# Kernel tuning notes

Measured on AMD Instinct MI355X. Metric: run time of the kernel, lower is better.

Reference implementation:

```python
import jax, jax.numpy as jnp
import numpy as np

# Sizes (see shape_source): N samples, D=Config.dim, H=D//2, E question types, C classes/type
N, D, H, E, C = 65536, 768, 384, 8, 8


def setup_inputs() -> dict:
    key = jax.random.key(0)
    k_x, k_t, k_w1, k_w2 = jax.random.split(key, 4)
    x = jax.random.normal(k_x, (N, D), dtype=jnp.float32)
    question_types = jax.random.randint(k_t, (N,), 0, E, dtype=jnp.int32)
    # Stacked per-type MLP head parameters (E experts)
    W1 = jax.random.normal(k_w1, (E, D, H), dtype=jnp.float32) * 0.02
    b1 = jnp.zeros((E, H), dtype=jnp.float32)
    W2 = jax.random.normal(k_w2, (E, H, C), dtype=jnp.float32) * 0.02
    b2 = jnp.zeros((E, C), dtype=jnp.float32)
    return {"x": x, "W1": W1, "b1": b1, "W2": W2, "b2": b2,
            "question_types": question_types}


def reference(x, W1, b1, W2, b2, question_types):
    # Per-sample routed 2-layer MLP head: logits_i = MLP_{type_i}(x_i).
    # Dropout is eval-mode identity. Dense-per-expert compute + mask select
    # (standard MoE reference; E is a small fixed loop, not a data-dim loop).
    n_experts = W1.shape[0]
    out = jnp.zeros((x.shape[0], W2.shape[-1]), dtype=x.dtype)
    for e in range(n_experts):
        h = jax.nn.relu(x @ W1[e] + b1[e])        # [N, H]
        logits = h @ W2[e] + b2[e]                # [N, C]
        out = jnp.where((question_types == e)[:, None], logits, out)
    return out
```

## Files before the change

kernel.cpp:

```cpp
#include <hip/hip_runtime.h>

typedef short s16x8 __attribute__((ext_vector_type(8)));
typedef float f32x4 __attribute__((ext_vector_type(4)));

#define N_SAMPLES 65536
#define DIM 768
#define HID 384
#define NEXP 8
#define NCLS 8
#define JT 24
#define KT 24

#define WS_CNT    0
#define WS_BUCKET 1024
#define WS_W1F    (WS_BUCKET + NEXP * N_SAMPLES * 4)

__device__ __forceinline__ unsigned short f2bf(float f) {
  union { float f; unsigned u; } v; v.f = f;
  unsigned r = v.u + 0x7fffu + ((v.u >> 16) & 1u);
  return (unsigned short)(r >> 16);
}

__device__ __forceinline__ unsigned cvt2(float a, float b) {
  union { float f; unsigned u; } ua, ub;
  ua.f = a; ub.f = b;
  return __builtin_amdgcn_perm(ub.u + 0x8000u, ua.u + 0x8000u, 0x07060302u);
}

#define LBAR asm volatile("s_waitcnt lgkmcnt(0)\n\ts_barrier" ::: "memory")

__global__ void k_w1frag(const float* __restrict__ W1,
                         unsigned short* __restrict__ W1F,
                         int* __restrict__ cnt) {
  if (blockIdx.x == 0 && blockIdx.y == 0 && threadIdx.x < NEXP)
    cnt[threadIdx.x] = 0;
  const int e = blockIdx.x;
  const int unit = blockIdx.y * 4 + (threadIdx.x >> 6);
  const int lane = threadIdx.x & 63;
  const int jt = unit / KT, kt = unit % KT;
  const int j = jt * 16 + (lane & 15);
  const int k0 = kt * 32 + (lane >> 4) * 8;
  const float* src = W1 + ((size_t)e * DIM + k0) * HID + j;
  s16x8 v;
#pragma unroll
  for (int i = 0; i < 8; ++i) v[i] = (short)f2bf(src[(size_t)i * HID]);
  *(s16x8*)&W1F[(((size_t)e * JT * KT + unit) * 64 + lane) * 8] = v;
}

__global__ void k_scatter(const int* __restrict__ qt, int* __restrict__ cnt,
                          int* __restrict__ bucket) {
  __shared__ int lcnt[NEXP], lbase[NEXP];
  const int t = threadIdx.x;
  const int i = blockIdx.x * 256 + t;
  if (t < NEXP) lcnt[t] = 0;
  __syncthreads();
  const int e = qt[i];
  const int rank = atomicAdd(&lcnt[e], 1);
  __syncthreads();
  if (t < NEXP) lbase[t] = atomicAdd(&cnt[t], lcnt[t]);
  __syncthreads();
  bucket[(size_t)e * N_SAMPLES + lbase[e] + rank] = i;
}

#define ALOAD(LO, HI, KS)                                   \
  { const float4* p_ = (const float4*)(ap + (KS) * 32);     \
    LO = p_[0]; HI = p_[1]; }

#define ASTORE(BUF, LO, HI)                                               \
  { unsigned q0 = cvt2((LO).x, (LO).y), q1 = cvt2((LO).z, (LO).w);        \
    unsigned q2 = cvt2((HI).x, (HI).y), q3 = cvt2((HI).z, (HI).w);        \
    uint4 pk_ = {q0, q1, q2, q3};                                         \
    *(uint4*)&(BUF)[ar * 40 + aq * 8] = pk_; }

#define WLOAD(DST, KS)                                                    \
  _Pragma("unroll") for (int ni = 0; ni < 6; ++ni)                        \
      DST[ni] = *(const s16x8*)(wfbase + ((size_t)ni * KT + (KS)) * 512);

#define COMPUTE(AS, WF)                                                   \
  { _Pragma("unroll") for (int mi = 0; mi < 4; ++mi) {                    \
      s16x8 xfr = *(const s16x8*)&(AS)[(mi * 16 + lrow) * 40 + quad * 8]; \
      _Pragma("unroll") for (int ni = 0; ni < 6; ++ni)                    \
          acc[mi][ni] = __builtin_amdgcn_mfma_f32_16x16x32_bf16(          \
              WF[ni], xfr, acc[mi][ni], 0, 0, 0); } }

__global__ __launch_bounds__(256, 2) void k_moe_gemm(
    const float* __restrict__ x, const unsigned short* __restrict__ W1F,
    const float* __restrict__ b1, const float* __restrict__ W2,
    const float* __restrict__ b2, const int* __restrict__ cnt,
    const int* __restrict__ bucket, float* __restrict__ out) {
  __shared__ __align__(16) short smem[25088];
  __shared__ __align__(16) short W2s[16 * 392];
  __shared__ float b1s[HID];
  __shared__ float b2s[NCLS];
  short* As0 = smem;
  short* As1 = smem + 2560;
  short* Hs  = smem;

  const int e = blockIdx.x;
  const int n_e = cnt[e];
  const int t = threadIdx.x;
  const int lane = t & 63;
  const int wave = t >> 6;
  const int lrow = lane & 15;
  const int quad = lane >> 4;
  const int ar = t >> 2;
  const int aq = t & 3;

  for (int j = t; j < HID; j += 256) {
    b1s[j] = b1[e * HID + j];
    const float* wr = W2 + ((size_t)e * HID + j) * NCLS;
#pragma unroll
    for (int c = 0; c < NCLS; ++c) W2s[c * 392 + j] = (short)f2bf(wr[c]);
#pragma unroll
    for (int c = NCLS; c < 16; ++c) W2s[c * 392 + j] = 0;
  }
  if (t < NCLS) b2s[t] = b2[e * NCLS + t];

  const unsigned short* wfbase =
      W1F + ((size_t)(e * JT + wave * 6) * KT) * 512 + lane * 8;

  for (int rt = blockIdx.y; rt * 64 < n_e; rt += gridDim.y) {
    const int row0 = rt * 64;
    int slot = row0 + ar;
    if (slot >= n_e) slot = n_e - 1;
    const int aidx = bucket[(size_t)e * N_SAMPLES + slot];
    const float* ap = x + (size_t)aidx * DIM + aq * 8;

    f32x4 acc[4][6];
#pragma unroll
    for (int mi = 0; mi < 4; ++mi)
#pragma unroll
      for (int ni = 0; ni < 6; ++ni) acc[mi][ni] = (f32x4){0.f, 0.f, 0.f, 0.f};

    float4 a0lo, a0hi, a1lo, a1hi;
    s16x8 wf0[6], wf1[6];
    ALOAD(a0lo, a0hi, 0)
    ASTORE(As0, a0lo, a0hi)
    ALOAD(a1lo, a1hi, 1)
    WLOAD(wf0, 0)
    LBAR;

    for (int ks = 0; ks < 24; ks += 2) {
      if (ks + 1 < 24) { ASTORE(As1, a1lo, a1hi) WLOAD(wf1, ks + 1) }
      if (ks + 2 < 24) ALOAD(a0lo, a0hi, ks + 2)
      COMPUTE(As0, wf0)
      LBAR;
      if (ks + 2 < 24) { ASTORE(As0, a0lo, a0hi) WLOAD(wf0, ks + 2) }
      if (ks + 3 < 24) ALOAD(a1lo, a1hi, ks + 3)
      COMPUTE(As1, wf1)
      LBAR;
    }

#pragma unroll
    for (int mi = 0; mi < 4; ++mi)
#pragma unroll
      for (int ni = 0; ni < 6; ++ni) {
        const int j = wave * 96 + ni * 16 + quad * 4;
        const float4 bb = *(const float4*)&b1s[j];
        float v0 = acc[mi][ni][0] + bb.x; v0 = v0 > 0.f ? v0 : 0.f;
        float v1 = acc[mi][ni][1] + bb.y; v1 = v1 > 0.f ? v1 : 0.f;
        float v2 = acc[mi][ni][2] + bb.z; v2 = v2 > 0.f ? v2 : 0.f;
        float v3 = acc[mi][ni][3] + bb.w; v3 = v3 > 0.f ? v3 : 0.f;
        uint2 pk = {cvt2(v0, v1), cvt2(v2, v3)};
        *(uint2*)&Hs[(mi * 16 + lrow) * 392 + j] = pk;
      }
    LBAR;

    {
      f32x4 acc2 = (f32x4){0.f, 0.f, 0.f, 0.f};
#pragma unroll
      for (int kk = 0; kk < 12; ++kk) {
        s16x8 af = *(const s16x8*)&Hs[(wave * 16 + lrow) * 392 + kk * 32 + quad * 8];
        s16x8 bf = *(const s16x8*)&W2s[lrow * 392 + kk * 32 + quad * 8];
        acc2 = __builtin_amdgcn_mfma_f32_16x16x32_bf16(af, bf, acc2, 0, 0, 0);
      }
      if (lrow < NCLS) {
        const float bb = b2s[lrow];
#pragma unroll
        for (int r = 0; r < 4; ++r) {
          const int m = wave * 16 + quad * 4 + r;
          if (row0 + m < n_e) {
            const int oi = bucket[(size_t)e * N_SAMPLES + row0 + m];
            out[(size_t)oi * NCLS + lrow] = acc2[r] + bb;
          }
        }
      }
    }
    LBAR;
  }
}

extern "C" void kernel_launch(void* const* d_in, const int* in_sizes, int n_in,
                              void* d_out, int out_size, void* d_ws, size_t ws_size,
                              hipStream_t stream) {
  const float* x  = (const float*)d_in[0];
  const float* W1 = (const float*)d_in[1];
  const float* b1 = (const float*)d_in[2];
  const float* W2 = (const float*)d_in[3];
  const float* b2 = (const float*)d_in[4];
  const int* qt   = (const int*)d_in[5];
  float* out = (float*)d_out;
  char* ws = (char*)d_ws;

  int* cnt = (int*)(ws + WS_CNT);
  int* bucket = (int*)(ws + WS_BUCKET);
  unsigned short* W1F = (unsigned short*)(ws + WS_W1F);

  k_w1frag<<<dim3(8, 144), dim3(256), 0, stream>>>(W1, W1F, cnt);
  k_scatter<<<dim3(256), dim3(256), 0, stream>>>(qt, cnt, bucket);
  k_moe_gemm<<<dim3(8, 64), dim3(256), 0, stream>>>(x, W1F, b1, W2, b2, cnt, bucket, out);
}
```

Baseline: 334.8 us.

## Load x fragments directly into registers, drop LDS staging, precompute W2 bf16

The main GEMM loop stops staging x tiles through shared memory. Each lane now gathers its own MFMA fragment rows straight from global memory into registers and converts them to bf16 in place, which removes the per-step LDS barriers. The W2 transpose and bf16 conversion move into extra blocks of the scatter kernel, and biases are read directly from global memory. Shared memory shrinks to the hidden buffer only and the grid grows from 64 to 144 row-tile blocks per expert. The cost is more register pressure from double-buffered float fragments, and the global reads are less coalesced: each lane fetches a 32-byte slice of a different row.

```diff
diff --git a/kernel.cpp b/kernel.cpp
--- a/kernel.cpp
+++ b/kernel.cpp
@@ -14,6 +14,7 @@
 #define WS_CNT    0
 #define WS_BUCKET 1024
 #define WS_W1F    (WS_BUCKET + NEXP * N_SAMPLES * 4)
+#define WS_W2T    (WS_W1F + NEXP * JT * KT * 64 * 8 * 2)
 
 __device__ __forceinline__ unsigned short f2bf(float f) {
   union { float f; unsigned u; } v; v.f = f;
@@ -47,10 +48,22 @@
   *(s16x8*)&W1F[(((size_t)e * JT * KT + unit) * 64 + lane) * 8] = v;
 }
 
-__global__ void k_scatter(const int* __restrict__ qt, int* __restrict__ cnt,
-                          int* __restrict__ bucket) {
+__global__ void k_scatter(const int* __restrict__ qt, const float* __restrict__ W2,
+                          int* __restrict__ cnt, int* __restrict__ bucket,
+                          unsigned short* __restrict__ W2T) {
+  const int t = threadIdx.x;
+  if (blockIdx.x >= 256) {
+    const int e = blockIdx.x - 256;
+    for (int j = t; j < HID; j += 256) {
+#pragma unroll
+      for (int c = 0; c < NCLS; ++c)
+        W2T[((size_t)e * 16 + c) * HID + j] = f2bf(W2[((size_t)e * HID + j) * NCLS + c]);
+#pragma unroll
+      for (int c = NCLS; c < 16; ++c) W2T[((size_t)e * 16 + c) * HID + j] = 0;
+    }
+    return;
+  }
   __shared__ int lcnt[NEXP], lbase[NEXP];
-  const int t = threadIdx.x;
   const int i = blockIdx.x * 256 + t;
   if (t < NEXP) lcnt[t] = 0;
   __syncthreads();
@@ -62,40 +75,34 @@
   bucket[(size_t)e * N_SAMPLES + lbase[e] + rank] = i;
 }
 
-#define ALOAD(LO, HI, KS)                                   \
-  { const float4* p_ = (const float4*)(ap + (KS) * 32);     \
-    LO = p_[0]; HI = p_[1]; }
-
-#define ASTORE(BUF, LO, HI)                                               \
-  { unsigned q0 = cvt2((LO).x, (LO).y), q1 = cvt2((LO).z, (LO).w);        \
-    unsigned q2 = cvt2((HI).x, (HI).y), q3 = cvt2((HI).z, (HI).w);        \
-    uint4 pk_ = {q0, q1, q2, q3};                                         \
-    *(uint4*)&(BUF)[ar * 40 + aq * 8] = pk_; }
+#define XLOAD(BUF, KS)                                                    \
+  _Pragma("unroll") for (int mi = 0; mi < 4; ++mi) {                      \
+    const float4* p_ = (const float4*)(xp[mi] + (KS) * 32);               \
+    BUF##lo[mi] = p_[0]; BUF##hi[mi] = p_[1];                             \
+  }
 
 #define WLOAD(DST, KS)                                                    \
   _Pragma("unroll") for (int ni = 0; ni < 6; ++ni)                        \
       DST[ni] = *(const s16x8*)(wfbase + ((size_t)ni * KT + (KS)) * 512);
 
-#define COMPUTE(AS, WF)                                                   \
-  { _Pragma("unroll") for (int mi = 0; mi < 4; ++mi) {                    \
-      s16x8 xfr = *(const s16x8*)&(AS)[(mi * 16 + lrow) * 40 + quad * 8]; \
-      _Pragma("unroll") for (int ni = 0; ni < 6; ++ni)                    \
-          acc[mi][ni] = __builtin_amdgcn_mfma_f32_16x16x32_bf16(          \
-              WF[ni], xfr, acc[mi][ni], 0, 0, 0); } }
+#define COMPUTE(XB, WF)                                                   \
+  _Pragma("unroll") for (int mi = 0; mi < 4; ++mi) {                      \
+    unsigned q0 = cvt2(XB##lo[mi].x, XB##lo[mi].y);                       \
+    unsigned q1 = cvt2(XB##lo[mi].z, XB##lo[mi].w);                       \
+    unsigned q2 = cvt2(XB##hi[mi].x, XB##hi[mi].y);                       \
+    unsigned q3 = cvt2(XB##hi[mi].z, XB##hi[mi].w);                       \
+    union { uint4 u; s16x8 s; } xf_; xf_.u = (uint4){q0, q1, q2, q3};     \
+    _Pragma("unroll") for (int ni = 0; ni < 6; ++ni)                      \
+        acc[mi][ni] = __builtin_amdgcn_mfma_f32_16x16x32_bf16(            \
+            WF[ni], xf_.s, acc[mi][ni], 0, 0, 0);                         \
+  }
 
 __global__ __launch_bounds__(256, 2) void k_moe_gemm(
     const float* __restrict__ x, const unsigned short* __restrict__ W1F,
-    const float* __restrict__ b1, const float* __restrict__ W2,
+    const float* __restrict__ b1, const unsigned short* __restrict__ W2T,
     const float* __restrict__ b2, const int* __restrict__ cnt,
     const int* __restrict__ bucket, float* __restrict__ out) {
-  __shared__ __align__(16) short smem[25088];
-  __shared__ __align__(16) short W2s[16 * 392];
-  __shared__ float b1s[HID];
-  __shared__ float b2s[NCLS];
-  short* As0 = smem;
-  short* As1 = smem + 2560;
-  short* Hs  = smem;
-
+  __shared__ __align__(16) short Hs[64 * 392];
   const int e = blockIdx.x;
   const int n_e = cnt[e];
   const int t = threadIdx.x;
@@ -103,28 +110,21 @@
   const int wave = t >> 6;
   const int lrow = lane & 15;
   const int quad = lane >> 4;
-  const int ar = t >> 2;
-  const int aq = t & 3;
-
-  for (int j = t; j < HID; j += 256) {
-    b1s[j] = b1[e * HID + j];
-    const float* wr = W2 + ((size_t)e * HID + j) * NCLS;
-#pragma unroll
-    for (int c = 0; c < NCLS; ++c) W2s[c * 392 + j] = (short)f2bf(wr[c]);
-#pragma unroll
-    for (int c = NCLS; c < 16; ++c) W2s[c * 392 + j] = 0;
-  }
-  if (t < NCLS) b2s[t] = b2[e * NCLS + t];
 
   const unsigned short* wfbase =
       W1F + ((size_t)(e * JT + wave * 6) * KT) * 512 + lane * 8;
 
   for (int rt = blockIdx.y; rt * 64 < n_e; rt += gridDim.y) {
     const int row0 = rt * 64;
-    int slot = row0 + ar;
-    if (slot >= n_e) slot = n_e - 1;
-    const int aidx = bucket[(size_t)e * N_SAMPLES + slot];
-    const float* ap = x + (size_t)aidx * DIM + aq * 8;
+    LBAR;
+
+    const float* xp[4];
+#pragma unroll
+    for (int mi = 0; mi < 4; ++mi) {
+      int slot = row0 + mi * 16 + lrow;
+      if (slot >= n_e) slot = n_e - 1;
+      xp[mi] = x + (size_t)bucket[(size_t)e * N_SAMPLES + slot] * DIM + quad * 8;
+    }
 
     f32x4 acc[4][6];
 #pragma unroll
@@ -132,50 +132,44 @@
 #pragma unroll
       for (int ni = 0; ni < 6; ++ni) acc[mi][ni] = (f32x4){0.f, 0.f, 0.f, 0.f};
 
-    float4 a0lo, a0hi, a1lo, a1hi;
-    s16x8 wf0[6], wf1[6];
-    ALOAD(a0lo, a0hi, 0)
-    ASTORE(As0, a0lo, a0hi)
-    ALOAD(a1lo, a1hi, 1)
-    WLOAD(wf0, 0)
-    LBAR;
+    float4 Alo[4], Ahi[4], Blo[4], Bhi[4];
+    s16x8 wfA[6], wfB[6];
+    XLOAD(A, 0) WLOAD(wfA, 0)
+    XLOAD(B, 1) WLOAD(wfB, 1)
 
     for (int ks = 0; ks < 24; ks += 2) {
-      if (ks + 1 < 24) { ASTORE(As1, a1lo, a1hi) WLOAD(wf1, ks + 1) }
-      if (ks + 2 < 24) ALOAD(a0lo, a0hi, ks + 2)
-      COMPUTE(As0, wf0)
-      LBAR;
-      if (ks + 2 < 24) { ASTORE(As0, a0lo, a0hi) WLOAD(wf0, ks + 2) }
-      if (ks + 3 < 24) ALOAD(a1lo, a1hi, ks + 3)
-      COMPUTE(As1, wf1)
-      LBAR;
-    }
-
-#pragma unroll
-    for (int mi = 0; mi < 4; ++mi)
-#pragma unroll
-      for (int ni = 0; ni < 6; ++ni) {
-        const int j = wave * 96 + ni * 16 + quad * 4;
-        const float4 bb = *(const float4*)&b1s[j];
+      COMPUTE(A, wfA)
+      if (ks + 2 < 24) { XLOAD(A, ks + 2) WLOAD(wfA, ks + 2) }
+      COMPUTE(B, wfB)
+      if (ks + 3 < 24) { XLOAD(B, ks + 3) WLOAD(wfB, ks + 3) }
+    }
+
+#pragma unroll
+    for (int ni = 0; ni < 6; ++ni) {
+      const float4 bb = *(const float4*)(b1 + e * HID + wave * 96 + ni * 16 + quad * 4);
+#pragma unroll
+      for (int mi = 0; mi < 4; ++mi) {
         float v0 = acc[mi][ni][0] + bb.x; v0 = v0 > 0.f ? v0 : 0.f;
         float v1 = acc[mi][ni][1] + bb.y; v1 = v1 > 0.f ? v1 : 0.f;
         float v2 = acc[mi][ni][2] + bb.z; v2 = v2 > 0.f ? v2 : 0.f;
         float v3 = acc[mi][ni][3] + bb.w; v3 = v3 > 0.f ? v3 : 0.f;
         uint2 pk = {cvt2(v0, v1), cvt2(v2, v3)};
-        *(uint2*)&Hs[(mi * 16 + lrow) * 392 + j] = pk;
+        *(uint2*)&Hs[(mi * 16 + lrow) * 392 + wave * 96 + ni * 16 + quad * 4] = pk;
       }
+    }
     LBAR;
 
     {
       f32x4 acc2 = (f32x4){0.f, 0.f, 0.f, 0.f};
+      const unsigned short* w2p = W2T + ((size_t)e * 16 + lrow) * HID + quad * 8;
 #pragma unroll
       for (int kk = 0; kk < 12; ++kk) {
         s16x8 af = *(const s16x8*)&Hs[(wave * 16 + lrow) * 392 + kk * 32 + quad * 8];
-        s16x8 bf = *(const s16x8*)&W2s[lrow * 392 + kk * 32 + quad * 8];
+        s16x8 bf = *(const s16x8*)(w2p + kk * 32);
         acc2 = __builtin_amdgcn_mfma_f32_16x16x32_bf16(af, bf, acc2, 0, 0, 0);
       }
       if (lrow < NCLS) {
-        const float bb = b2s[lrow];
+        const float bb = b2[e * NCLS + lrow];
 #pragma unroll
         for (int r = 0; r < 4; ++r) {
           const int m = wave * 16 + quad * 4 + r;
@@ -186,7 +180,6 @@
         }
       }
     }
-    LBAR;
   }
 }
 
@@ -205,8 +198,9 @@
   int* cnt = (int*)(ws + WS_CNT);
   int* bucket = (int*)(ws + WS_BUCKET);
   unsigned short* W1F = (unsigned short*)(ws + WS_W1F);
+  unsigned short* W2T = (unsigned short*)(ws + WS_W2T);
 
   k_w1frag<<<dim3(8, 144), dim3(256), 0, stream>>>(W1, W1F, cnt);
-  k_scatter<<<dim3(256), dim3(256), 0, stream>>>(qt, cnt, bucket);
-  k_moe_gemm<<<dim3(8, 64), dim3(256), 0, stream>>>(x, W1F, b1, W2, b2, cnt, bucket, out);
-}
+  k_scatter<<<dim3(264), dim3(256), 0, stream>>>(qt, W2, cnt, bucket, W2T);
+  k_moe_gemm<<<dim3(8, 144), dim3(256), 0, stream>>>(x, W1F, b1, W2T, b2, cnt, bucket, out);
+}
```

Result: slower. 407.7 us (+21.8%).
